# Kernel optimization log

Measured on AMD Instinct MI355X. Metric: run time of the kernel, lower is better.

The kernel has to match this reference:

```python
import jax, jax.numpy as jnp
import numpy as np


def setup_inputs() -> dict:
    key = jax.random.key(0)
    ks = jax.random.split(key, 9)
    N_POI, N_TIME, D = 10000, 48, 500
    S, L = 2048, 4096  # state_len (cur), seq_len (his)
    return {
        "his": jax.random.randint(ks[0], (L,), 0, N_POI, dtype=jnp.int32),
        "cur": jax.random.randint(ks[1], (S,), 0, N_POI, dtype=jnp.int32),
        "his_t": jax.random.randint(ks[2], (L,), 0, N_TIME, dtype=jnp.int32),
        "cur_t": jax.random.randint(ks[3], (S,), 0, N_TIME, dtype=jnp.int32),
        "poi_distance_mat": jax.random.uniform(ks[4], (N_POI, N_POI), dtype=jnp.float32),
        "time_sim_mat": jax.random.uniform(ks[5], (N_TIME, N_TIME), dtype=jnp.float32),
        "user_emb": jax.random.normal(ks[6], (S, D), dtype=jnp.float32),
        "id_emb": jax.random.normal(ks[7], (L, D), dtype=jnp.float32),
        "socail_uid_emb": jax.random.normal(ks[8], (D,), dtype=jnp.float32),
        "w1_socail": jnp.float32(0.6),
        "w2_socail": jnp.float32(0.4),
    }


def reference(his, cur, his_t, cur_t, poi_distance_mat, time_sim_mat,
              user_emb, id_emb, socail_uid_emb, w1_socail, w2_socail):
    # Attn_loc: energies[i,j] = 1/dist[cur[i],his[j]] if nonzero else 1e-6
    d = poi_distance_mat[cur[:, None], his[None, :]]          # [S, L] gather
    nz = d != 0
    loc_energy = jnp.where(nz, 1.0 / jnp.where(nz, d, 1.0), 1e-6)
    attn_loc = jax.nn.softmax(loc_energy, axis=-1)

    # Attn_time: energies[i,j] = time_sim[cur_t[i], his_t[j]]
    time_energy = time_sim_mat[cur_t[:, None], his_t[None, :]]  # [S, L]
    attn_time = jax.nn.softmax(time_energy, axis=-1)

    # Attn_user ('dot'): w1 * <user_emb[i], id_emb[j]> + w2 * <socail, id_emb[j]>
    user_energy = (w1_socail * jnp.einsum('sd,ld->sl', user_emb, id_emb)
                   + w2_socail * (id_emb @ socail_uid_emb)[None, :])  # [S, L]
    attn_user = jax.nn.softmax(user_energy, axis=-1)

    return jnp.stack([attn_loc, attn_time, attn_user])  # [3, S, L]
```

## Files before the change

kernel.cpp:

```cpp
#include <hip/hip_runtime.h>
#include <math.h>

#define S_DIM 2048
#define L_DIM 4096
#define D_DIM 500
#define KPAD 512
#define NPOI 10000
#define NTIME 48

typedef __attribute__((ext_vector_type(8))) short short8;
typedef __attribute__((ext_vector_type(4))) float f32x4;
typedef __attribute__((ext_vector_type(16))) float f32x16;

__device__ __forceinline__ float wave_max(float v) {
#pragma unroll
  for (int o = 32; o > 0; o >>= 1) v = fmaxf(v, __shfl_down(v, o, 64));
  return v;
}
__device__ __forceinline__ float wave_sum(float v) {
#pragma unroll
  for (int o = 32; o > 0; o >>= 1) v += __shfl_down(v, o, 64);
  return v;
}
__device__ __forceinline__ short f2bf(float x) {
  union { float f; unsigned u; } v;
  v.f = x;
  const unsigned r = v.u + 0x7fffu + ((v.u >> 16) & 1u);
  return (short)(r >> 16);
}
__device__ __forceinline__ float bf2f(short h) {
  union { unsigned u; float f; } v;
  v.u = ((unsigned)(unsigned short)h) << 16;
  return v.f;
}

__global__ __launch_bounds__(256) void attn_loc_kernel(
    const int* __restrict__ cur, const int* __restrict__ his,
    const float* __restrict__ poi, float* __restrict__ out) {
  __shared__ float rowbuf[NPOI];
  __shared__ float redm[4];
  __shared__ float reds[4];
  const int s = blockIdx.x;
  const int tid = threadIdx.x;
  const float* row = poi + (size_t)cur[s] * NPOI;
  for (int i = tid; i < NPOI / 4; i += 256)
    *reinterpret_cast<float4*>(&rowbuf[i * 4]) =
        *reinterpret_cast<const float4*>(row + i * 4);
  __syncthreads();
  float v[16];
  float lmax = -1e30f;
#pragma unroll
  for (int j = 0; j < 16; ++j) {
    const int l = j * 256 + tid;
    const float d = rowbuf[his[l]];
    const float e = (d != 0.0f) ? (1.0f / d) : 1e-6f;
    v[j] = e;
    lmax = fmaxf(lmax, e);
  }
  lmax = wave_max(lmax);
  if ((tid & 63) == 0) redm[tid >> 6] = lmax;
  __syncthreads();
  const float m = fmaxf(fmaxf(redm[0], redm[1]), fmaxf(redm[2], redm[3]));
  float lsum = 0.f;
#pragma unroll
  for (int j = 0; j < 16; ++j) {
    v[j] = __expf(v[j] - m);
    lsum += v[j];
  }
  lsum = wave_sum(lsum);
  if ((tid & 63) == 0) reds[tid >> 6] = lsum;
  __syncthreads();
  const float inv = 1.0f / (reds[0] + reds[1] + reds[2] + reds[3]);
  float* o = out + (size_t)s * L_DIM;
#pragma unroll
  for (int j = 0; j < 16; ++j) o[j * 256 + tid] = v[j] * inv;
}

__global__ __launch_bounds__(256) void time_table_kernel(
    const int* __restrict__ his_t, const float* __restrict__ T,
    float* __restrict__ P) {
  __shared__ int cnt[NTIME];
  __shared__ float Ts[NTIME * NTIME];
  const int tid = threadIdx.x;
  if (tid < NTIME) cnt[tid] = 0;
  __syncthreads();
  for (int l = tid; l < L_DIM; l += 256) atomicAdd(&cnt[his_t[l]], 1);
  for (int i = tid; i < NTIME * NTIME; i += 256) Ts[i] = T[i];
  __syncthreads();
  if (tid < NTIME) {
    float m = -1e30f;
    for (int t = 0; t < NTIME; ++t) m = fmaxf(m, Ts[tid * NTIME + t]);
    float den = 0.f;
    for (int t = 0; t < NTIME; ++t)
      den += (float)cnt[t] * __expf(Ts[tid * NTIME + t] - m);
    const float inv = 1.0f / den;
    for (int t = 0; t < NTIME; ++t)
      P[tid * NTIME + t] = __expf(Ts[tid * NTIME + t] - m) * inv;
  }
}

__global__ __launch_bounds__(256) void time_out_kernel(
    const int* __restrict__ cur_t, const int* __restrict__ his_t,
    const float* __restrict__ P, float* __restrict__ out) {
  const int i = blockIdx.x * 256 + threadIdx.x;
  const int s = i >> 12;
  const int l = i & (L_DIM - 1);
  out[i] = P[cur_t[s] * NTIME + his_t[l]];
}

__global__ __launch_bounds__(256) void split_kernel(
    const float* __restrict__ U, const float* __restrict__ Id,
    const float* __restrict__ w1p, const float* __restrict__ soc,
    const float* __restrict__ w2p, short* __restrict__ planes,
    float* __restrict__ bias) {
  const int chunk = blockIdx.x * 256 + threadIdx.x;
  const int row = chunk >> 6;
  const int lq = chunk & 63;
  const bool isA = row < S_DIM;
  const float scale = isA ? w1p[0] : 1.0f;
  const float* src = isA ? (U + (size_t)row * D_DIM)
                         : (Id + (size_t)(row - S_DIM) * D_DIM);
  const int k0 = lq * 8;
  float dot = 0.f;
  short h[8], l[8];
#pragma unroll
  for (int e = 0; e < 8; ++e) {
    const int k = k0 + e;
    const float v = (k < D_DIM) ? src[k] : 0.0f;
    if (!isA && k < D_DIM) dot += v * soc[k];
    const float x = scale * v;
    const short hb = f2bf(x);
    h[e] = hb;
    l[e] = f2bf(x - bf2f(hb));
  }
  const int rb = row >> 7, rin = row & 127;
  const int ks = lq >> 2, kq = lq & 3;
  const int off = rin * 64 + ((kq ^ ((rin >> 1) & 3)) * 16);
  char* base = (char*)planes + ((size_t)(rb * 16 + ks) * 2) * 8192;
  *reinterpret_cast<int4*>(base + off) = *reinterpret_cast<const int4*>(h);
  *reinterpret_cast<int4*>(base + 8192 + off) =
      *reinterpret_cast<const int4*>(l);
  if (!isA) {
    const float d = wave_sum(dot);
    if ((threadIdx.x & 63) == 0) bias[row - S_DIM] = w2p[0] * d;
  }
}

__global__ __launch_bounds__(256, 2) void user_gemm_mfma(
    const short* __restrict__ planes, const float* __restrict__ bias,
    float* __restrict__ outE) {
  __shared__ __attribute__((aligned(1024))) char lds[32768];
  const int tid = threadIdx.x;
  const int lane = tid & 63;
  const int wid = tid >> 6;
  const int wm = (wid >> 1) * 64;
  const int wn = (wid & 1) * 64;
  const int bm = blockIdx.y * 128;
  const int bn = blockIdx.x * 128;
  const int arb = blockIdx.y;
  const int brb = 16 + blockIdx.x;
  const char* gA = (const char*)planes + (size_t)arb * 16 * 2 * 8192;
  const char* gB = (const char*)planes + (size_t)brb * 16 * 2 * 8192;

  const int r32 = lane & 31;
  const int khl = lane >> 5;

  f32x16 acc[2][2] = {};

  for (int ks = 0; ks < KPAD / 32; ++ks) {
    const char* tA = gA + (size_t)ks * 16384;
    const char* tB = gB + (size_t)ks * 16384;
#pragma unroll
    for (int q = 0; q < 4; ++q) {
      const int c = (q * 256 + tid) * 16;
      __builtin_amdgcn_global_load_lds(
          (const __attribute__((address_space(1))) unsigned int*)(tA + c),
          (__attribute__((address_space(3))) unsigned int*)(lds + c), 16, 0, 0);
      __builtin_amdgcn_global_load_lds(
          (const __attribute__((address_space(1))) unsigned int*)(tB + c),
          (__attribute__((address_space(3))) unsigned int*)(lds + 16384 + c),
          16, 0, 0);
    }
    __syncthreads();
#pragma unroll
    for (int kf = 0; kf < 2; ++kf) {
      short8 ah[2], al[2], bh[2], bl[2];
#pragma unroll
      for (int i = 0; i < 2; ++i) {
        const int ra = wm + i * 32 + r32;
        const int rb_ = wn + i * 32 + r32;
        const int ga = ((kf * 2 + khl) ^ ((ra >> 1) & 3)) * 16;
        const int gb = ((kf * 2 + khl) ^ ((rb_ >> 1) & 3)) * 16;
        ah[i] = *reinterpret_cast<const short8*>(lds + ra * 64 + ga);
        al[i] = *reinterpret_cast<const short8*>(lds + 8192 + ra * 64 + ga);
        bh[i] = *reinterpret_cast<const short8*>(lds + 16384 + rb_ * 64 + gb);
        bl[i] = *reinterpret_cast<const short8*>(lds + 24576 + rb_ * 64 + gb);
      }
#pragma unroll
      for (int i = 0; i < 2; ++i)
#pragma unroll
        for (int j = 0; j < 2; ++j) {
          acc[i][j] = __builtin_amdgcn_mfma_f32_32x32x16_bf16(
              ah[i], bh[j], acc[i][j], 0, 0, 0);
          acc[i][j] = __builtin_amdgcn_mfma_f32_32x32x16_bf16(
              ah[i], bl[j], acc[i][j], 0, 0, 0);
          acc[i][j] = __builtin_amdgcn_mfma_f32_32x32x16_bf16(
              al[i], bh[j], acc[i][j], 0, 0, 0);
        }
    }
    __syncthreads();
  }

#pragma unroll
  for (int j = 0; j < 2; ++j) {
    const int col = bn + wn + j * 32 + r32;
    const float bj = bias[col];
#pragma unroll
    for (int i = 0; i < 2; ++i) {
      const int rbase = bm + wm + i * 32 + 4 * khl;
#pragma unroll
      for (int reg = 0; reg < 16; ++reg) {
        const int rowm = rbase + (reg & 3) + 8 * (reg >> 2);
        outE[(size_t)rowm * L_DIM + col] = acc[i][j][reg] + bj;
      }
    }
  }
}

__global__ __launch_bounds__(256) void user_softmax_kernel(
    float* __restrict__ outE) {
  __shared__ float redm[4];
  __shared__ float reds[4];
  const int s = blockIdx.x;
  const int tid = threadIdx.x;
  float* row = outE + (size_t)s * L_DIM;
  float4 v[4];
  float lmax = -1e30f;
#pragma unroll
  for (int j = 0; j < 4; ++j) {
    v[j] = *reinterpret_cast<const float4*>(&row[(j * 256 + tid) * 4]);
    lmax = fmaxf(lmax, fmaxf(fmaxf(v[j].x, v[j].y), fmaxf(v[j].z, v[j].w)));
  }
  lmax = wave_max(lmax);
  if ((tid & 63) == 0) redm[tid >> 6] = lmax;
  __syncthreads();
  const float m = fmaxf(fmaxf(redm[0], redm[1]), fmaxf(redm[2], redm[3]));
  float lsum = 0.f;
#pragma unroll
  for (int j = 0; j < 4; ++j) {
    v[j].x = __expf(v[j].x - m);
    v[j].y = __expf(v[j].y - m);
    v[j].z = __expf(v[j].z - m);
    v[j].w = __expf(v[j].w - m);
    lsum += v[j].x + v[j].y + v[j].z + v[j].w;
  }
  lsum = wave_sum(lsum);
  if ((tid & 63) == 0) reds[tid >> 6] = lsum;
  __syncthreads();
  const float inv = 1.0f / (reds[0] + reds[1] + reds[2] + reds[3]);
#pragma unroll
  for (int j = 0; j < 4; ++j) {
    v[j].x *= inv;
    v[j].y *= inv;
    v[j].z *= inv;
    v[j].w *= inv;
    *reinterpret_cast<float4*>(&row[(j * 256 + tid) * 4]) = v[j];
  }
}

extern "C" void kernel_launch(void* const* d_in, const int* in_sizes, int n_in,
                              void* d_out, int out_size, void* d_ws,
                              size_t ws_size, hipStream_t stream) {
  const int* his = (const int*)d_in[0];
  const int* cur = (const int*)d_in[1];
  const int* his_t = (const int*)d_in[2];
  const int* cur_t = (const int*)d_in[3];
  const float* poi = (const float*)d_in[4];
  const float* tsim = (const float*)d_in[5];
  const float* uemb = (const float*)d_in[6];
  const float* idemb = (const float*)d_in[7];
  const float* soc = (const float*)d_in[8];
  const float* w1 = (const float*)d_in[9];
  const float* w2 = (const float*)d_in[10];

  float* out = (float*)d_out;
  float* out_loc = out;
  float* out_time = out + (size_t)S_DIM * L_DIM;
  float* out_user = out + 2 * (size_t)S_DIM * L_DIM;

  const size_t plane_bytes = (size_t)48 * 16 * 2 * 8192;
  short* planes;
  float* bias;
  float* P;
  if (ws_size >= plane_bytes + 32768) {
    planes = (short*)d_ws;
    bias = (float*)((char*)d_ws + plane_bytes);
    P = bias + L_DIM;
  } else {
    planes = (short*)out_loc;
    bias = (float*)d_ws;
    P = bias + L_DIM;
  }

  hipLaunchKernelGGL(split_kernel, dim3((S_DIM + L_DIM) * 64 / 256), dim3(256),
                     0, stream, uemb, idemb, w1, soc, w2, planes, bias);
  hipLaunchKernelGGL(user_gemm_mfma, dim3(L_DIM / 128, S_DIM / 128), dim3(256),
                     0, stream, planes, bias, out_user);
  hipLaunchKernelGGL(user_softmax_kernel, dim3(S_DIM), dim3(256), 0, stream,
                     out_user);
  hipLaunchKernelGGL(time_table_kernel, dim3(1), dim3(256), 0, stream, his_t,
                     tsim, P);
  hipLaunchKernelGGL(time_out_kernel, dim3((S_DIM * L_DIM) / 256), dim3(256),
                     0, stream, cur_t, his_t, P, out_time);
  hipLaunchKernelGGL(attn_loc_kernel, dim3(S_DIM), dim3(256), 0, stream, cur,
                     his, poi, out_loc);
}
```

Baseline: 104.1 us.

## Fuse time output into loc kernel; double-buffer larger-tile MFMA GEMM

The time-attention output write moves into the location softmax kernel, so one launch and a separate index-gather pass are removed. The user GEMM now uses 256x128 tiles with 512 threads, double-buffered LDS staging that prefetches the next K slice during compute, a new XOR swizzle, and a block-index remap for L2 locality. The split kernel writes a matching plane layout. In exchange, LDS use per block rises and the combined kernel does more work per block.

Measured after the change: 88.59 us. -14.9%, faster.

```diff
diff --git a/kernel.cpp b/kernel.cpp
--- a/kernel.cpp
+++ b/kernel.cpp
@@ -9,8 +9,11 @@
 #define NTIME 48
 
 typedef __attribute__((ext_vector_type(8))) short short8;
-typedef __attribute__((ext_vector_type(4))) float f32x4;
 typedef __attribute__((ext_vector_type(16))) float f32x16;
+
+#define A_BYTES 4194304
+#define PLANE_BYTES 12582912
+#define LDSBUF 49152
 
 __device__ __forceinline__ float wave_max(float v) {
 #pragma unroll
@@ -34,14 +37,18 @@
   return v.f;
 }
 
-__global__ __launch_bounds__(256) void attn_loc_kernel(
+__global__ __launch_bounds__(256) void attn_loc_time_kernel(
     const int* __restrict__ cur, const int* __restrict__ his,
-    const float* __restrict__ poi, float* __restrict__ out) {
-  __shared__ float rowbuf[NPOI];
+    const float* __restrict__ poi, const int* __restrict__ cur_t,
+    const int* __restrict__ his_t, const float* __restrict__ P,
+    float* __restrict__ out_loc, float* __restrict__ out_time) {
+  __shared__ __attribute__((aligned(16))) float rowbuf[NPOI];
+  __shared__ float Prow[NTIME];
   __shared__ float redm[4];
   __shared__ float reds[4];
   const int s = blockIdx.x;
   const int tid = threadIdx.x;
+  if (tid < NTIME) Prow[tid] = P[cur_t[s] * NTIME + tid];
   const float* row = poi + (size_t)cur[s] * NPOI;
   for (int i = tid; i < NPOI / 4; i += 256)
     *reinterpret_cast<float4*>(&rowbuf[i * 4]) =
@@ -71,9 +78,14 @@
   if ((tid & 63) == 0) reds[tid >> 6] = lsum;
   __syncthreads();
   const float inv = 1.0f / (reds[0] + reds[1] + reds[2] + reds[3]);
-  float* o = out + (size_t)s * L_DIM;
-#pragma unroll
-  for (int j = 0; j < 16; ++j) o[j * 256 + tid] = v[j] * inv;
+  float* ol = out_loc + (size_t)s * L_DIM;
+  float* ot = out_time + (size_t)s * L_DIM;
+#pragma unroll
+  for (int j = 0; j < 16; ++j) {
+    const int l = j * 256 + tid;
+    ol[l] = v[j] * inv;
+    ot[l] = Prow[his_t[l]];
+  }
 }
 
 __global__ __launch_bounds__(256) void time_table_kernel(
@@ -97,15 +109,6 @@
     for (int t = 0; t < NTIME; ++t)
       P[tid * NTIME + t] = __expf(Ts[tid * NTIME + t] - m) * inv;
   }
-}
-
-__global__ __launch_bounds__(256) void time_out_kernel(
-    const int* __restrict__ cur_t, const int* __restrict__ his_t,
-    const float* __restrict__ P, float* __restrict__ out) {
-  const int i = blockIdx.x * 256 + threadIdx.x;
-  const int s = i >> 12;
-  const int l = i & (L_DIM - 1);
-  out[i] = P[cur_t[s] * NTIME + his_t[l]];
 }
 
 __global__ __launch_bounds__(256) void split_kernel(
@@ -133,68 +136,89 @@
     h[e] = hb;
     l[e] = f2bf(x - bf2f(hb));
   }
-  const int rb = row >> 7, rin = row & 127;
-  const int ks = lq >> 2, kq = lq & 3;
-  const int off = rin * 64 + ((kq ^ ((rin >> 1) & 3)) * 16);
-  char* base = (char*)planes + ((size_t)(rb * 16 + ks) * 2) * 8192;
-  *reinterpret_cast<int4*>(base + off) = *reinterpret_cast<const int4*>(h);
-  *reinterpret_cast<int4*>(base + 8192 + off) =
-      *reinterpret_cast<const int4*>(l);
-  if (!isA) {
+  const int ks = lq >> 2, g = lq & 3;
+  if (isA) {
+    const int mb = row >> 8, rin = row & 255;
+    const int gs = g ^ (rin & 3) ^ ((rin >> 2) & 3);
+    char* base = (char*)planes + (size_t)(mb * 16 + ks) * 32768 + rin * 64 +
+                 gs * 16;
+    *reinterpret_cast<int4*>(base) = *reinterpret_cast<const int4*>(h);
+    *reinterpret_cast<int4*>(base + 16384) = *reinterpret_cast<const int4*>(l);
+  } else {
+    const int rb = row - S_DIM;
+    const int nb = rb >> 7, rin = rb & 127;
+    const int gs = g ^ (rin & 3) ^ ((rin >> 2) & 3);
+    char* base = (char*)planes + A_BYTES + (size_t)(nb * 16 + ks) * 16384 +
+                 rin * 64 + gs * 16;
+    *reinterpret_cast<int4*>(base) = *reinterpret_cast<const int4*>(h);
+    *reinterpret_cast<int4*>(base + 8192) = *reinterpret_cast<const int4*>(l);
     const float d = wave_sum(dot);
-    if ((threadIdx.x & 63) == 0) bias[row - S_DIM] = w2p[0] * d;
-  }
-}
-
-__global__ __launch_bounds__(256, 2) void user_gemm_mfma(
+    if ((threadIdx.x & 63) == 0) bias[rb] = w2p[0] * d;
+  }
+}
+
+__global__ __launch_bounds__(512, 2) void user_gemm_mfma(
     const short* __restrict__ planes, const float* __restrict__ bias,
     float* __restrict__ outE) {
-  __shared__ __attribute__((aligned(1024))) char lds[32768];
+  __shared__ __attribute__((aligned(1024))) char lds[2 * LDSBUF];
   const int tid = threadIdx.x;
   const int lane = tid & 63;
   const int wid = tid >> 6;
+  const int ob = (blockIdx.x & 7) * 32 + (blockIdx.x >> 3);
+  const int nb = ob >> 3;
+  const int mb = ob & 7;
+  const int bm = mb * 256, bn = nb * 128;
+  const char* gA = (const char*)planes + (size_t)mb * 16 * 32768;
+  const char* gB = (const char*)planes + A_BYTES + (size_t)nb * 16 * 16384;
   const int wm = (wid >> 1) * 64;
   const int wn = (wid & 1) * 64;
-  const int bm = blockIdx.y * 128;
-  const int bn = blockIdx.x * 128;
-  const int arb = blockIdx.y;
-  const int brb = 16 + blockIdx.x;
-  const char* gA = (const char*)planes + (size_t)arb * 16 * 2 * 8192;
-  const char* gB = (const char*)planes + (size_t)brb * 16 * 2 * 8192;
-
   const int r32 = lane & 31;
   const int khl = lane >> 5;
 
   f32x16 acc[2][2] = {};
 
-  for (int ks = 0; ks < KPAD / 32; ++ks) {
-    const char* tA = gA + (size_t)ks * 16384;
-    const char* tB = gB + (size_t)ks * 16384;
-#pragma unroll
-    for (int q = 0; q < 4; ++q) {
-      const int c = (q * 256 + tid) * 16;
-      __builtin_amdgcn_global_load_lds(
-          (const __attribute__((address_space(1))) unsigned int*)(tA + c),
-          (__attribute__((address_space(3))) unsigned int*)(lds + c), 16, 0, 0);
-      __builtin_amdgcn_global_load_lds(
-          (const __attribute__((address_space(1))) unsigned int*)(tB + c),
-          (__attribute__((address_space(3))) unsigned int*)(lds + 16384 + c),
-          16, 0, 0);
-    }
-    __syncthreads();
-#pragma unroll
-    for (int kf = 0; kf < 2; ++kf) {
+#define STAGE(ks_, buf_)                                                      \
+  {                                                                           \
+    const int _ks = (ks_);                                                    \
+    char* _dst = lds + (buf_)*LDSBUF;                                         \
+    _Pragma("unroll") for (int q = 0; q < 6; ++q) {                           \
+      const int off = (q * 512 + tid) * 16;                                   \
+      if (q < 4) {                                                            \
+        __builtin_amdgcn_global_load_lds(                                     \
+            (const __attribute__((address_space(1))) unsigned*)(gA +          \
+                (size_t)_ks * 32768 + off),                                   \
+            (__attribute__((address_space(3))) unsigned*)(_dst + off), 16, 0, \
+            0);                                                               \
+      } else {                                                                \
+        __builtin_amdgcn_global_load_lds(                                     \
+            (const __attribute__((address_space(1))) unsigned*)(gB +          \
+                (size_t)_ks * 16384 + (off - 32768)),                         \
+            (__attribute__((address_space(3))) unsigned*)(_dst + off), 16, 0, \
+            0);                                                               \
+      }                                                                       \
+    }                                                                         \
+  }
+
+  STAGE(0, 0);
+  __syncthreads();
+  int buf = 0;
+  for (int ks = 0; ks < 16; ++ks) {
+    if (ks < 15) STAGE(ks + 1, buf ^ 1);
+    const char* La = lds + buf * LDSBUF;
+    const char* Lb = La + 32768;
+#pragma unroll
+    for (int s16 = 0; s16 < 2; ++s16) {
       short8 ah[2], al[2], bh[2], bl[2];
 #pragma unroll
       for (int i = 0; i < 2; ++i) {
         const int ra = wm + i * 32 + r32;
-        const int rb_ = wn + i * 32 + r32;
-        const int ga = ((kf * 2 + khl) ^ ((ra >> 1) & 3)) * 16;
-        const int gb = ((kf * 2 + khl) ^ ((rb_ >> 1) & 3)) * 16;
-        ah[i] = *reinterpret_cast<const short8*>(lds + ra * 64 + ga);
-        al[i] = *reinterpret_cast<const short8*>(lds + 8192 + ra * 64 + ga);
-        bh[i] = *reinterpret_cast<const short8*>(lds + 16384 + rb_ * 64 + gb);
-        bl[i] = *reinterpret_cast<const short8*>(lds + 24576 + rb_ * 64 + gb);
+        const int ga = ((s16 * 2 + khl) ^ (ra & 3) ^ ((ra >> 2) & 3)) * 16;
+        ah[i] = *reinterpret_cast<const short8*>(La + ra * 64 + ga);
+        al[i] = *reinterpret_cast<const short8*>(La + 16384 + ra * 64 + ga);
+        const int rbb = wn + i * 32 + r32;
+        const int gb = ((s16 * 2 + khl) ^ (rbb & 3) ^ ((rbb >> 2) & 3)) * 16;
+        bh[i] = *reinterpret_cast<const short8*>(Lb + rbb * 64 + gb);
+        bl[i] = *reinterpret_cast<const short8*>(Lb + 8192 + rbb * 64 + gb);
       }
 #pragma unroll
       for (int i = 0; i < 2; ++i)
@@ -209,15 +233,18 @@
         }
     }
     __syncthreads();
-  }
-
+    buf ^= 1;
+  }
+#undef STAGE
+
+  const int rg = 4 * khl;
 #pragma unroll
   for (int j = 0; j < 2; ++j) {
     const int col = bn + wn + j * 32 + r32;
     const float bj = bias[col];
 #pragma unroll
     for (int i = 0; i < 2; ++i) {
-      const int rbase = bm + wm + i * 32 + 4 * khl;
+      const int rbase = bm + wm + i * 32 + rg;
 #pragma unroll
       for (int reg = 0; reg < 16; ++reg) {
         const int rowm = rbase + (reg & 3) + 8 * (reg >> 2);
@@ -288,13 +315,12 @@
   float* out_time = out + (size_t)S_DIM * L_DIM;
   float* out_user = out + 2 * (size_t)S_DIM * L_DIM;
 
-  const size_t plane_bytes = (size_t)48 * 16 * 2 * 8192;
   short* planes;
   float* bias;
   float* P;
-  if (ws_size >= plane_bytes + 32768) {
+  if (ws_size >= (size_t)PLANE_BYTES + 32768) {
     planes = (short*)d_ws;
-    bias = (float*)((char*)d_ws + plane_bytes);
+    bias = (float*)((char*)d_ws + PLANE_BYTES);
     P = bias + L_DIM;
   } else {
     planes = (short*)out_loc;
@@ -304,14 +330,12 @@
 
   hipLaunchKernelGGL(split_kernel, dim3((S_DIM + L_DIM) * 64 / 256), dim3(256),
                      0, stream, uemb, idemb, w1, soc, w2, planes, bias);
-  hipLaunchKernelGGL(user_gemm_mfma, dim3(L_DIM / 128, S_DIM / 128), dim3(256),
-                     0, stream, planes, bias, out_user);
+  hipLaunchKernelGGL(time_table_kernel, dim3(1), dim3(256), 0, stream, his_t,
+                     tsim, P);
+  hipLaunchKernelGGL(user_gemm_mfma, dim3(256), dim3(512), 0, stream, planes,
+                     bias, out_user);
   hipLaunchKernelGGL(user_softmax_kernel, dim3(S_DIM), dim3(256), 0, stream,
                      out_user);
-  hipLaunchKernelGGL(time_table_kernel, dim3(1), dim3(256), 0, stream, his_t,
-                     tsim, P);
-  hipLaunchKernelGGL(time_out_kernel, dim3((S_DIM * L_DIM) / 256), dim3(256),
-                     0, stream, cur_t, his_t, P, out_time);
-  hipLaunchKernelGGL(attn_loc_kernel, dim3(S_DIM), dim3(256), 0, stream, cur,
-                     his, poi, out_loc);
-}
+  hipLaunchKernelGGL(attn_loc_time_kernel, dim3(S_DIM), dim3(256), 0, stream,
+                     cur, his, poi, cur_t, his_t, P, out_loc, out_time);
+}
```
